# Optimization experiments

Hardware: AMD Instinct MI355X
Metric: run time of the kernel (lower is better)

## Reference

```python
import jax, jax.numpy as jnp
import numpy as np

N_NODES = 32
GAT_OUT = 64
LSTM_H = 128
N_CLS = 4
NEG_SLOPE = 0.2


def setup_inputs() -> dict:
    key = jax.random.key(0)
    ks = jax.random.split(key, 12)
    B, T, E = 32, 512, 96
    F, H = GAT_OUT, LSTM_H
    s = 0.05
    return {
        "x_seq": jax.random.normal(ks[0], (B, T, N_NODES), jnp.float32),
        "edge_index": jax.random.randint(ks[1], (2, E), 0, N_NODES, jnp.int32),
        # GATConv params (heads=1): lin weight [in=1, F], attention vectors [F], bias [F]
        "w_gat": jax.random.normal(ks[2], (1, F), jnp.float32) * s,
        "att_src": jax.random.normal(ks[3], (F,), jnp.float32) * s,
        "att_dst": jax.random.normal(ks[4], (F,), jnp.float32) * s,
        "b_gat": jnp.zeros((F,), jnp.float32),
        # LSTM params, torch gate order (i, f, g, o)
        "W_ih": jax.random.normal(ks[5], (N_NODES * F, 4 * H), jnp.float32) * s,
        "W_hh": jax.random.normal(ks[6], (H, 4 * H), jnp.float32) * s,
        "b_ih": jnp.zeros((4 * H,), jnp.float32),
        "b_hh": jnp.zeros((4 * H,), jnp.float32),
        # classifier
        "W_fc": jax.random.normal(ks[7], (H, N_CLS), jnp.float32) * s,
        "b_fc": jnp.zeros((N_CLS,), jnp.float32),
    }


def _forward(x_seq, edge_index, w_gat, att_src, att_dst, b_gat,
             W_ih, W_hh, b_ih, b_hh, W_fc, b_fc):
    B, T, N = x_seq.shape
    F = w_gat.shape[1]
    H = W_hh.shape[0]

    # --- GAT over all (B,T) steps at once (PyG GATConv, heads=1, self-loops) ---
    loops = jnp.arange(N, dtype=edge_index.dtype)
    src = jnp.concatenate([edge_index[0], loops])  # [Et]
    dst = jnp.concatenate([edge_index[1], loops])  # [Et]
    Et = src.shape[0]

    h = x_seq[..., None] * w_gat            # [B,T,N,F] (in_channels=1 linear)
    a_s = h @ att_src                        # [B,T,N]
    a_d = h @ att_dst                        # [B,T,N]
    e = a_s[..., src] + a_d[..., dst]        # [B,T,Et]
    e = jnp.where(e > 0, e, NEG_SLOPE * e)   # LeakyReLU(0.2)

    # segment softmax over destination node, batched over B*T
    e2 = jnp.moveaxis(e, -1, 0).reshape(Et, B * T)
    m = jax.ops.segment_max(e2, dst, num_segments=N)        # [N,B*T]
    ex = jnp.exp(e2 - m[dst])
    z = jax.ops.segment_sum(ex, dst, num_segments=N)        # [N,B*T]
    alpha = ex / z[dst]                                      # [Et,B*T]
    alpha = jnp.moveaxis(alpha.reshape(Et, B, T), 0, -1)     # [B,T,Et]

    msg = alpha[..., None] * h[:, :, src, :]                 # [B,T,Et,F]
    onehot = (dst[:, None] == jnp.arange(N)).astype(h.dtype)  # [Et,N]
    out = jnp.einsum('btef,en->btnf', msg, onehot) + b_gat    # [B,T,N,F]

    seq = out.reshape(B, T, N * F)           # [B,T,2048]

    # --- single-layer LSTM (batch_first), torch gate order i,f,g,o ---
    xw = seq @ W_ih + (b_ih + b_hh)          # [B,T,4H]

    def step(carry, xw_t):
        hs, cs = carry
        g = xw_t + hs @ W_hh                 # [B,4H]
        i, f, gg, o = jnp.split(g, 4, axis=-1)
        cs = jax.nn.sigmoid(f) * cs + jax.nn.sigmoid(i) * jnp.tanh(gg)
        hs = jax.nn.sigmoid(o) * jnp.tanh(cs)
        return (hs, cs), None

    h0 = jnp.zeros((B, H), seq.dtype)
    (h_last, _), _ = jax.lax.scan(step, (h0, h0), jnp.moveaxis(xw, 1, 0))

    return h_last @ W_fc + b_fc              # [B,num_classes]


def reference(x_seq, edge_index, w_gat, att_src, att_dst, b_gat,
              W_ih, W_hh, b_ih, b_hh, W_fc, b_fc):
    return _forward(x_seq, edge_index, w_gat, att_src, att_dst, b_gat,
                    W_ih, W_hh, b_ih, b_hh, W_fc, b_fc)
```

## Files before the change

### kernel.cpp

```cpp
#include <hip/hip_runtime.h>

#define NN 32
#define FF 64
#define HH 128
#define G4 512
#define BB 32
#define TT 512
#define ET 128
#define NPOS (BB*TT)

__device__ __forceinline__ float frcp(float x) { return __builtin_amdgcn_rcpf(x); }

__global__ __launch_bounds__(512) void prep_kernel(const float* __restrict__ w_gat,
                                                   const float* __restrict__ b_gat,
                                                   const float* __restrict__ W_ih,
                                                   float* __restrict__ W_eff,
                                                   float* __restrict__ biasp) {
  int j = threadIdx.x;
  int n = blockIdx.x;
  float accw = 0.f, accb = 0.f;
#pragma unroll 8
  for (int f = 0; f < FF; ++f) {
    float wv = W_ih[(n * FF + f) * G4 + j];
    accw = fmaf(w_gat[f], wv, accw);
    accb = fmaf(b_gat[f], wv, accb);
  }
  W_eff[n * G4 + j] = accw;
  biasp[n * G4 + j] = accb;
}

__global__ __launch_bounds__(512) void prep2_kernel(const float* __restrict__ biasp,
                                                    const float* __restrict__ b_ih,
                                                    const float* __restrict__ b_hh,
                                                    const float* __restrict__ w_gat,
                                                    const float* __restrict__ att_src,
                                                    const float* __restrict__ att_dst,
                                                    const int* __restrict__ ei,
                                                    float* __restrict__ bias_eff,
                                                    float* __restrict__ scal,
                                                    int* __restrict__ srt_g,
                                                    int* __restrict__ off_g) {
  __shared__ int cnt[NN];
  __shared__ int off[NN + 1];
  __shared__ int srt[ET];
  int j = threadIdx.x;
  if (j < NN) cnt[j] = 0;
  float acc = b_ih[j] + b_hh[j];
#pragma unroll
  for (int n = 0; n < NN; ++n) acc += biasp[n * G4 + j];
  bias_eff[j] = acc;
  if (j == 0) {
    float cs = 0.f, cd = 0.f;
    for (int f = 0; f < FF; ++f) {
      cs = fmaf(w_gat[f], att_src[f], cs);
      cd = fmaf(w_gat[f], att_dst[f], cd);
    }
    scal[0] = cs;
    scal[1] = cd;
  }
  __syncthreads();
  int s = 0, d = 0, tk = 0;
  if (j < ET) {
    if (j < 96) { s = ei[j]; d = ei[96 + j]; }
    else { s = j - 96; d = j - 96; }
    tk = atomicAdd(&cnt[d], 1);
  }
  __syncthreads();
  if (j == 0) {
    off[0] = 0;
    for (int n = 0; n < NN; ++n) off[n + 1] = off[n] + cnt[n];
  }
  __syncthreads();
  if (j < ET) srt[off[d] + tk] = s;
  __syncthreads();
  if (j < ET) srt_g[j] = srt[j];
  if (j < NN + 1) off_g[j] = off[j];
}

__global__ __launch_bounds__(128) void prep3_kernel(const float* __restrict__ W_hh,
                                                    float* __restrict__ Wt) {
  int tid = blockIdx.x;
  int m = threadIdx.x;
  int r = tid >> 2, kq = tid & 3;
  int g = m >> 5, kk = m & 31;
  Wt[tid * 128 + m] = W_hh[(kq * 32 + kk) * G4 + g * 128 + r];
}

__global__ __launch_bounds__(256) void gatxw_kernel(const float* __restrict__ x_seq,
                                                    const int* __restrict__ srt_g,
                                                    const int* __restrict__ off_g,
                                                    const float* __restrict__ scal,
                                                    const float* __restrict__ W_eff,
                                                    const float* __restrict__ bias_eff,
                                                    float* __restrict__ xw) {
  __shared__ int srt[ET];
  __shared__ int offs[NN + 1];
  __shared__ float xs[8 * 32];
  __shared__ float sl[8 * 32];
  int tid = threadIdx.x;
  int posbase = blockIdx.x * 8;
  float we0[NN], we1[NN];
#pragma unroll
  for (int nn = 0; nn < NN; ++nn) {
    we0[nn] = W_eff[nn * G4 + tid];
    we1[nn] = W_eff[nn * G4 + 256 + tid];
  }
  float b0 = bias_eff[tid], b1 = bias_eff[256 + tid];
  if (tid < ET) srt[tid] = srt_g[tid];
  if (tid < NN + 1) offs[tid] = off_g[tid];
  int p = tid >> 5, n = tid & 31;
  xs[tid] = x_seq[posbase * NN + tid];
  __syncthreads();
  float cs = scal[0], cd = scal[1];
  int base = p * 32;
  int e0 = offs[n], e1 = offs[n + 1];
  float xn = xs[base + n];
  float cdxn = cd * xn;
  float m = -3.0e38f;
  for (int e = e0; e < e1; ++e) {
    float ev = fmaf(cs, xs[base + srt[e]], cdxn);
    ev = ev > 0.f ? ev : 0.2f * ev;
    m = fmaxf(m, ev);
  }
  float z = 0.f, sa = 0.f;
  for (int e = e0; e < e1; ++e) {
    float xsv = xs[base + srt[e]];
    float ev = fmaf(cs, xsv, cdxn);
    ev = ev > 0.f ? ev : 0.2f * ev;
    float ex = __expf(ev - m);
    z += ex;
    sa = fmaf(ex, xsv, sa);
  }
  sl[p * 32 + n] = sa * frcp(z);
  __syncthreads();
  for (int pp = 0; pp < 8; ++pp) {
    const float4* sp = (const float4*)&sl[pp * 32];
    float a0 = b0, a1 = b1;
#pragma unroll
    for (int q = 0; q < 8; ++q) {
      float4 sv = sp[q];
      a0 = fmaf(sv.x, we0[4 * q], a0);
      a0 = fmaf(sv.y, we0[4 * q + 1], a0);
      a0 = fmaf(sv.z, we0[4 * q + 2], a0);
      a0 = fmaf(sv.w, we0[4 * q + 3], a0);
      a1 = fmaf(sv.x, we1[4 * q], a1);
      a1 = fmaf(sv.y, we1[4 * q + 1], a1);
      a1 = fmaf(sv.z, we1[4 * q + 2], a1);
      a1 = fmaf(sv.w, we1[4 * q + 3], a1);
    }
    size_t row = (size_t)(posbase + pp) * G4;
    xw[row + tid] = a0;
    xw[row + 256 + tid] = a1;
  }
}


#define PK16F(HP, W0, W1, W2, W3) \
  "v_pk_fma_f32 v[216:217], v[" HP "], v[" W0 "], 0\n\t" \
  "v_pk_fma_f32 v[218:219], v[" HP "], v[" W1 "], 0\n\t" \
  "v_pk_fma_f32 v[220:221], v[" HP "], v[" W2 "], 0\n\t" \
  "v_pk_fma_f32 v[222:223], v[" HP "], v[" W3 "], 0\n\t"

#define PK16A(HP, W0, W1, W2, W3) \
  "v_pk_fma_f32 v[216:217], v[" HP "], v[" W0 "], v[216:217]\n\t" \
  "v_pk_fma_f32 v[218:219], v[" HP "], v[" W1 "], v[218:219]\n\t" \
  "v_pk_fma_f32 v[220:221], v[" HP "], v[" W2 "], v[220:221]\n\t" \
  "v_pk_fma_f32 v[222:223], v[" HP "], v[" W3 "], v[222:223]\n\t"

#define PHASE(XSLOT, RD, WR) \
  "ds_read_b128 v[32:35], " RD "\n\t" \
  "ds_read_b128 v[36:39], " RD " offset:16\n\t" \
  "ds_read_b128 v[40:43], " RD " offset:32\n\t" \
  "ds_read_b128 v[44:47], " RD " offset:48\n\t" \
  "ds_read_b128 v[48:51], " RD " offset:64\n\t" \
  "ds_read_b128 v[52:55], " RD " offset:80\n\t" \
  "ds_read_b128 v[56:59], " RD " offset:96\n\t" \
  "ds_read_b128 v[60:63], " RD " offset:112\n\t" \
  "s_waitcnt vmcnt(3)\n\t" \
  "v_mov_b32 v215, " XSLOT "\n\t" \
  "global_load_dword " XSLOT ", v194, %[xwb]\n\t" \
  "v_add_u32 v194, 0x800, v194\n\t" \
  "s_waitcnt lgkmcnt(7)\n\t" \
  PK16F("32:33", "64:65",  "96:97",   "128:129", "160:161") \
  PK16A("34:35", "66:67",  "98:99",   "130:131", "162:163") \
  "s_waitcnt lgkmcnt(6)\n\t" \
  PK16A("36:37", "68:69",  "100:101", "132:133", "164:165") \
  PK16A("38:39", "70:71",  "102:103", "134:135", "166:167") \
  "s_waitcnt lgkmcnt(5)\n\t" \
  PK16A("40:41", "72:73",  "104:105", "136:137", "168:169") \
  PK16A("42:43", "74:75",  "106:107", "138:139", "170:171") \
  "s_waitcnt lgkmcnt(4)\n\t" \
  PK16A("44:45", "76:77",  "108:109", "140:141", "172:173") \
  PK16A("46:47", "78:79",  "110:111", "142:143", "174:175") \
  "s_waitcnt lgkmcnt(3)\n\t" \
  PK16A("48:49", "80:81",  "112:113", "144:145", "176:177") \
  PK16A("50:51", "82:83",  "114:115", "146:147", "178:179") \
  "s_waitcnt lgkmcnt(2)\n\t" \
  PK16A("52:53", "84:85",  "116:117", "148:149", "180:181") \
  PK16A("54:55", "86:87",  "118:119", "150:151", "182:183") \
  "s_waitcnt lgkmcnt(1)\n\t" \
  PK16A("56:57", "88:89",  "120:121", "152:153", "184:185") \
  PK16A("58:59", "90:91",  "122:123", "154:155", "186:187") \
  "s_waitcnt lgkmcnt(0)\n\t" \
  PK16A("60:61", "92:93",  "124:125", "156:157", "188:189") \
  PK16A("62:63", "94:95",  "126:127", "158:159", "190:191") \
  "v_add_f32 v204, v216, v217\n\t" \
  "v_add_f32 v205, v218, v219\n\t" \
  "v_add_f32 v206, v220, v221\n\t" \
  "v_add_f32 v207, v222, v223\n\t" \
  "v_fmac_f32 v204, v215, v200\n\t" \
  "v_fmac_f32 v205, v215, v201\n\t" \
  "v_fmac_f32 v206, v215, v202\n\t" \
  "v_fmac_f32 v207, v215, v203\n\t" \
  "v_add_f32_dpp v204, v204, v204 quad_perm:[1,0,3,2] row_mask:0xf bank_mask:0xf\n\t" \
  "v_add_f32_dpp v205, v205, v205 quad_perm:[1,0,3,2] row_mask:0xf bank_mask:0xf\n\t" \
  "v_add_f32_dpp v206, v206, v206 quad_perm:[1,0,3,2] row_mask:0xf bank_mask:0xf\n\t" \
  "v_add_f32_dpp v207, v207, v207 quad_perm:[1,0,3,2] row_mask:0xf bank_mask:0xf\n\t" \
  "v_add_f32_dpp v204, v204, v204 quad_perm:[2,3,0,1] row_mask:0xf bank_mask:0xf\n\t" \
  "v_add_f32_dpp v205, v205, v205 quad_perm:[2,3,0,1] row_mask:0xf bank_mask:0xf\n\t" \
  "v_add_f32_dpp v206, v206, v206 quad_perm:[2,3,0,1] row_mask:0xf bank_mask:0xf\n\t" \
  "v_add_f32_dpp v207, v207, v207 quad_perm:[2,3,0,1] row_mask:0xf bank_mask:0xf\n\t" \
  "v_mul_f32 v208, 0xbfb8aa3b, v204\n\t" \
  "v_mul_f32 v209, 0xbfb8aa3b, v205\n\t" \
  "v_mul_f32 v210, 0x4038aa3b, v206\n\t" \
  "v_mul_f32 v211, 0xbfb8aa3b, v207\n\t" \
  "v_exp_f32 v208, v208\n\t" \
  "v_exp_f32 v209, v209\n\t" \
  "v_exp_f32 v210, v210\n\t" \
  "v_exp_f32 v211, v211\n\t" \
  "v_add_f32 v208, 1.0, v208\n\t" \
  "v_add_f32 v209, 1.0, v209\n\t" \
  "v_add_f32 v210, 1.0, v210\n\t" \
  "v_add_f32 v211, 1.0, v211\n\t" \
  "v_rcp_f32 v208, v208\n\t" \
  "v_rcp_f32 v209, v209\n\t" \
  "v_rcp_f32 v210, v210\n\t" \
  "v_rcp_f32 v211, v211\n\t" \
  "v_fma_f32 v210, -2.0, v210, 1.0\n\t" \
  "v_mul_f32 v212, v208, v210\n\t" \
  "v_fma_f32 v199, v209, v199, v212\n\t" \
  "v_mul_f32 v214, 0x4038aa3b, v199\n\t" \
  "v_exp_f32 v214, v214\n\t" \
  "s_nop 1\n\t" \
  "v_add_f32 v214, 1.0, v214\n\t" \
  "v_rcp_f32 v214, v214\n\t" \
  "s_nop 1\n\t" \
  "v_fma_f32 v214, -2.0, v214, 1.0\n\t" \
  "v_mul_f32 v213, v211, v214\n\t" \
  "ds_write_b32 " WR ", v213\n\t" \
  "s_waitcnt lgkmcnt(0)\n\t" \
  "s_barrier\n\t"

__global__ __launch_bounds__(512, 2) void lstm_kernel(const float* __restrict__ xw,
                                                      const float* __restrict__ Wt,
                                                      const float* __restrict__ W_fc,
                                                      const float* __restrict__ b_fc,
                                                      float* __restrict__ out) {
  __shared__ __align__(16) float lds[320];
  int b = blockIdx.x, tid = threadIdx.x;
  int r = tid >> 2, kq = tid & 3;
  if (tid < 320) lds[tid] = 0.f;
  const float* xwb = xw + (size_t)b * TT * G4;
  unsigned xoff0 = (unsigned)((kq * 128 + r) * 4);
  unsigned wtoff = (unsigned)(tid * 512);
  unsigned lbase = (unsigned)(uintptr_t)&lds[0];
  unsigned rda = lbase + kq * 160;
  unsigned rdb = rda + 640;
  unsigned wra = lbase + (((r >> 5) * 40 + (r & 31)) << 2);
  unsigned wrb = wra + 640;
  float mh0 = (kq == 0) ? 1.f : 0.f;
  float mh1 = (kq == 1) ? 1.f : 0.f;
  float mh2 = (kq == 2) ? 1.f : 0.f;
  float mh3 = (kq == 3) ? 1.f : 0.f;
  __syncthreads();
  asm volatile(
    "v_mov_b32 v194, %[xo]\n\t"
    "v_mov_b32 v195, %[rda]\n\t"
    "v_mov_b32 v196, %[rdb]\n\t"
    "v_mov_b32 v197, %[wra]\n\t"
    "v_mov_b32 v198, %[wrb]\n\t"
    "v_mov_b32 v199, 0\n\t"
    "v_mov_b32 v200, %[m0]\n\t"
    "v_mov_b32 v201, %[m1]\n\t"
    "v_mov_b32 v202, %[m2]\n\t"
    "v_mov_b32 v203, %[m3]\n\t"
    "global_load_dword v224, v194, %[xwb]\n\t"
    "v_add_u32 v194, 0x800, v194\n\t"
    "global_load_dword v225, v194, %[xwb]\n\t"
    "v_add_u32 v194, 0x800, v194\n\t"
    "global_load_dword v226, v194, %[xwb]\n\t"
    "v_add_u32 v194, 0x800, v194\n\t"
    "global_load_dword v227, v194, %[xwb]\n\t"
    "v_add_u32 v194, 0x800, v194\n\t"
    "global_load_dwordx4 v[64:67], %[wto], %[wtb] offset:0\n\t"
    "global_load_dwordx4 v[68:71], %[wto], %[wtb] offset:16\n\t"
    "global_load_dwordx4 v[72:75], %[wto], %[wtb] offset:32\n\t"
    "global_load_dwordx4 v[76:79], %[wto], %[wtb] offset:48\n\t"
    "global_load_dwordx4 v[80:83], %[wto], %[wtb] offset:64\n\t"
    "global_load_dwordx4 v[84:87], %[wto], %[wtb] offset:80\n\t"
    "global_load_dwordx4 v[88:91], %[wto], %[wtb] offset:96\n\t"
    "global_load_dwordx4 v[92:95], %[wto], %[wtb] offset:112\n\t"
    "global_load_dwordx4 v[96:99], %[wto], %[wtb] offset:128\n\t"
    "global_load_dwordx4 v[100:103], %[wto], %[wtb] offset:144\n\t"
    "global_load_dwordx4 v[104:107], %[wto], %[wtb] offset:160\n\t"
    "global_load_dwordx4 v[108:111], %[wto], %[wtb] offset:176\n\t"
    "global_load_dwordx4 v[112:115], %[wto], %[wtb] offset:192\n\t"
    "global_load_dwordx4 v[116:119], %[wto], %[wtb] offset:208\n\t"
    "global_load_dwordx4 v[120:123], %[wto], %[wtb] offset:224\n\t"
    "global_load_dwordx4 v[124:127], %[wto], %[wtb] offset:240\n\t"
    "global_load_dwordx4 v[128:131], %[wto], %[wtb] offset:256\n\t"
    "global_load_dwordx4 v[132:135], %[wto], %[wtb] offset:272\n\t"
    "global_load_dwordx4 v[136:139], %[wto], %[wtb] offset:288\n\t"
    "global_load_dwordx4 v[140:143], %[wto], %[wtb] offset:304\n\t"
    "global_load_dwordx4 v[144:147], %[wto], %[wtb] offset:320\n\t"
    "global_load_dwordx4 v[148:151], %[wto], %[wtb] offset:336\n\t"
    "global_load_dwordx4 v[152:155], %[wto], %[wtb] offset:352\n\t"
    "global_load_dwordx4 v[156:159], %[wto], %[wtb] offset:368\n\t"
    "global_load_dwordx4 v[160:163], %[wto], %[wtb] offset:384\n\t"
    "global_load_dwordx4 v[164:167], %[wto], %[wtb] offset:400\n\t"
    "global_load_dwordx4 v[168:171], %[wto], %[wtb] offset:416\n\t"
    "global_load_dwordx4 v[172:175], %[wto], %[wtb] offset:432\n\t"
    "global_load_dwordx4 v[176:179], %[wto], %[wtb] offset:448\n\t"
    "global_load_dwordx4 v[180:183], %[wto], %[wtb] offset:464\n\t"
    "global_load_dwordx4 v[184:187], %[wto], %[wtb] offset:480\n\t"
    "global_load_dwordx4 v[188:191], %[wto], %[wtb] offset:496\n\t"
    "s_waitcnt vmcnt(4)\n\t"
    "s_movk_i32 s20, 0x80\n\t"
    "L_lstm_%=:\n\t"
    PHASE("v224", "v195", "v198")
    PHASE("v225", "v196", "v197")
    PHASE("v226", "v195", "v198")
    PHASE("v227", "v196", "v197")
    "s_sub_u32 s20, s20, 1\n\t"
    "s_cmp_lg_u32 s20, 0\n\t"
    "s_cbranch_scc1 L_lstm_%=\n\t"
    "s_waitcnt vmcnt(0) lgkmcnt(0)\n\t"
    :
    : [xwb]"s"(xwb), [wtb]"s"(Wt), [wto]"v"(wtoff), [xo]"v"(xoff0),
      [rda]"v"(rda), [rdb]"v"(rdb), [wra]"v"(wra), [wrb]"v"(wrb),
      [m0]"v"(mh0), [m1]"v"(mh1), [m2]"v"(mh2), [m3]"v"(mh3)
    : "memory", "scc", "s20",
      "v32","v33","v34","v35","v36","v37","v38","v39",
      "v40","v41","v42","v43","v44","v45","v46","v47",
      "v48","v49","v50","v51","v52","v53","v54","v55",
      "v56","v57","v58","v59","v60","v61","v62","v63",
      "v64","v65","v66","v67","v68","v69","v70","v71",
      "v72","v73","v74","v75","v76","v77","v78","v79",
      "v80","v81","v82","v83","v84","v85","v86","v87",
      "v88","v89","v90","v91","v92","v93","v94","v95",
      "v96","v97","v98","v99","v100","v101","v102","v103",
      "v104","v105","v106","v107","v108","v109","v110","v111",
      "v112","v113","v114","v115","v116","v117","v118","v119",
      "v120","v121","v122","v123","v124","v125","v126","v127",
      "v128","v129","v130","v131","v132","v133","v134","v135",
      "v136","v137","v138","v139","v140","v141","v142","v143",
      "v144","v145","v146","v147","v148","v149","v150","v151",
      "v152","v153","v154","v155","v156","v157","v158","v159",
      "v160","v161","v162","v163","v164","v165","v166","v167",
      "v168","v169","v170","v171","v172","v173","v174","v175",
      "v176","v177","v178","v179","v180","v181","v182","v183",
      "v184","v185","v186","v187","v188","v189","v190","v191",
      "v192","v193","v194","v195","v196","v197","v198","v199",
      "v200","v201","v202","v203","v204","v205","v206","v207",
      "v208","v209","v210","v211","v212","v213","v214","v215",
      "v216","v217","v218","v219","v220","v221","v222","v223",
      "v224","v225","v226","v227");
  __syncthreads();
  if (tid < 4) {
    float acc = b_fc[tid];
#pragma unroll 8
    for (int k = 0; k < HH; ++k)
      acc = fmaf(lds[(k >> 5) * 40 + (k & 31)], W_fc[k * 4 + tid], acc);
    out[b * 4 + tid] = acc;
  }
}

extern "C" void kernel_launch(void* const* d_in, const int* in_sizes, int n_in,
                              void* d_out, int out_size, void* d_ws, size_t ws_size,
                              hipStream_t stream) {
  const float* x_seq   = (const float*)d_in[0];
  const int*   ei      = (const int*)d_in[1];
  const float* w_gat   = (const float*)d_in[2];
  const float* att_src = (const float*)d_in[3];
  const float* att_dst = (const float*)d_in[4];
  const float* b_gat   = (const float*)d_in[5];
  const float* W_ih    = (const float*)d_in[6];
  const float* W_hh    = (const float*)d_in[7];
  const float* b_ih    = (const float*)d_in[8];
  const float* b_hh    = (const float*)d_in[9];
  const float* W_fc    = (const float*)d_in[10];
  const float* b_fc    = (const float*)d_in[11];

  float* ws = (float*)d_ws;
  float* Wt       = ws;
  float* xw       = Wt + 65536;
  float* W_eff    = xw + (size_t)(NPOS + 8) * G4;
  float* bias_eff = W_eff + NN * G4;
  float* scal     = bias_eff + G4;
  float* biasp    = scal + 2;
  int*   srt_g    = (int*)(biasp + NN * G4);
  int*   off_g    = srt_g + ET;

  prep_kernel<<<NN, G4, 0, stream>>>(w_gat, b_gat, W_ih, W_eff, biasp);
  prep2_kernel<<<1, G4, 0, stream>>>(biasp, b_ih, b_hh, w_gat, att_src, att_dst, ei,
                                     bias_eff, scal, srt_g, off_g);
  prep3_kernel<<<G4, 128, 0, stream>>>(W_hh, Wt);
  gatxw_kernel<<<NPOS / 8, 256, 0, stream>>>(x_seq, srt_g, off_g, scal, W_eff, bias_eff, xw);
  lstm_kernel<<<BB, G4, 0, stream>>>(xw, Wt, W_fc, b_fc, (float*)d_out);
}
```

Baseline: 396.1 us.

## Split LSTM K-reduction eight ways per hidden-unit pair and merge prep kernels

The LSTM recurrence now gives each thread two hidden units and an eighth of the K dimension, reduced with three DPP steps, instead of one unit and a quarter of K. This halves the per-thread shared-memory reads of h per step and shortens the serial FMA chain in the latency-bound recurrent loop, at the cost of an extra DPP stage and a reordered W_hh layout. The separate prep2/prep3 kernels are folded into prep_kernel and gatxw_kernel, which removes two launches but makes every gatxw block redo the edge sort, bias sum and attention scalars.

```diff
diff --git a/kernel.cpp b/kernel.cpp
--- a/kernel.cpp
+++ b/kernel.cpp
@@ -14,8 +14,10 @@
 __global__ __launch_bounds__(512) void prep_kernel(const float* __restrict__ w_gat,
                                                    const float* __restrict__ b_gat,
                                                    const float* __restrict__ W_ih,
+                                                   const float* __restrict__ W_hh,
                                                    float* __restrict__ W_eff,
-                                                   float* __restrict__ biasp) {
+                                                   float* __restrict__ biasp,
+                                                   float* __restrict__ Wt) {
   int j = threadIdx.x;
   int n = blockIdx.x;
   float accw = 0.f, accb = 0.f;
@@ -27,76 +29,34 @@
   }
   W_eff[n * G4 + j] = accw;
   biasp[n * G4 + j] = accb;
+  int g0 = (n * G4 + j) * 4;
+#pragma unroll
+  for (int q = 0; q < 4; ++q) {
+    int e = g0 + q;
+    int t = e >> 7, idx = e & 127;
+    int ko = t & 7, r2 = t >> 3;
+    int m = idx >> 4, kk = idx & 15;
+    int col = (m >> 1) * 128 + 2 * r2 + (m & 1);
+    Wt[e] = W_hh[(ko * 16 + kk) * G4 + col];
+  }
 }
 
-__global__ __launch_bounds__(512) void prep2_kernel(const float* __restrict__ biasp,
-                                                    const float* __restrict__ b_ih,
-                                                    const float* __restrict__ b_hh,
+__global__ __launch_bounds__(256) void gatxw_kernel(const float* __restrict__ x_seq,
+                                                    const int* __restrict__ ei,
                                                     const float* __restrict__ w_gat,
                                                     const float* __restrict__ att_src,
                                                     const float* __restrict__ att_dst,
-                                                    const int* __restrict__ ei,
-                                                    float* __restrict__ bias_eff,
-                                                    float* __restrict__ scal,
-                                                    int* __restrict__ srt_g,
-                                                    int* __restrict__ off_g) {
-  __shared__ int cnt[NN];
-  __shared__ int off[NN + 1];
-  __shared__ int srt[ET];
-  int j = threadIdx.x;
-  if (j < NN) cnt[j] = 0;
-  float acc = b_ih[j] + b_hh[j];
-#pragma unroll
-  for (int n = 0; n < NN; ++n) acc += biasp[n * G4 + j];
-  bias_eff[j] = acc;
-  if (j == 0) {
-    float cs = 0.f, cd = 0.f;
-    for (int f = 0; f < FF; ++f) {
-      cs = fmaf(w_gat[f], att_src[f], cs);
-      cd = fmaf(w_gat[f], att_dst[f], cd);
-    }
-    scal[0] = cs;
-    scal[1] = cd;
-  }
-  __syncthreads();
-  int s = 0, d = 0, tk = 0;
-  if (j < ET) {
-    if (j < 96) { s = ei[j]; d = ei[96 + j]; }
-    else { s = j - 96; d = j - 96; }
-    tk = atomicAdd(&cnt[d], 1);
-  }
-  __syncthreads();
-  if (j == 0) {
-    off[0] = 0;
-    for (int n = 0; n < NN; ++n) off[n + 1] = off[n] + cnt[n];
-  }
-  __syncthreads();
-  if (j < ET) srt[off[d] + tk] = s;
-  __syncthreads();
-  if (j < ET) srt_g[j] = srt[j];
-  if (j < NN + 1) off_g[j] = off[j];
-}
-
-__global__ __launch_bounds__(128) void prep3_kernel(const float* __restrict__ W_hh,
-                                                    float* __restrict__ Wt) {
-  int tid = blockIdx.x;
-  int m = threadIdx.x;
-  int r = tid >> 2, kq = tid & 3;
-  int g = m >> 5, kk = m & 31;
-  Wt[tid * 128 + m] = W_hh[(kq * 32 + kk) * G4 + g * 128 + r];
-}
-
-__global__ __launch_bounds__(256) void gatxw_kernel(const float* __restrict__ x_seq,
-                                                    const int* __restrict__ srt_g,
-                                                    const int* __restrict__ off_g,
-                                                    const float* __restrict__ scal,
+                                                    const float* __restrict__ b_ih,
+                                                    const float* __restrict__ b_hh,
                                                     const float* __restrict__ W_eff,
-                                                    const float* __restrict__ bias_eff,
+                                                    const float* __restrict__ biasp,
                                                     float* __restrict__ xw) {
   __shared__ int srt[ET];
   __shared__ int offs[NN + 1];
-  __shared__ float xs[8 * 32];
-  __shared__ float sl[8 * 32];
+  __shared__ int cnt[NN];
+  __shared__ float xs[256];
+  __shared__ float sl[256];
+  __shared__ float scal_sh[2];
   int tid = threadIdx.x;
   int posbase = blockIdx.x * 8;
   float we0[NN], we1[NN];
@@ -105,13 +65,41 @@
     we0[nn] = W_eff[nn * G4 + tid];
     we1[nn] = W_eff[nn * G4 + 256 + tid];
   }
-  float b0 = bias_eff[tid], b1 = bias_eff[256 + tid];
-  if (tid < ET) srt[tid] = srt_g[tid];
-  if (tid < NN + 1) offs[tid] = off_g[tid];
+  float b0 = b_ih[tid] + b_hh[tid];
+  float b1 = b_ih[256 + tid] + b_hh[256 + tid];
+#pragma unroll 8
+  for (int n = 0; n < NN; ++n) {
+    b0 += biasp[n * G4 + tid];
+    b1 += biasp[n * G4 + 256 + tid];
+  }
+  if (tid < NN) cnt[tid] = 0;
+  __syncthreads();
+  int es = 0, ed = 0, tk = 0;
+  if (tid < ET) {
+    if (tid < 96) { es = ei[tid]; ed = ei[96 + tid]; }
+    else { es = tid - 96; ed = tid - 96; }
+    tk = atomicAdd(&cnt[ed], 1);
+  }
+  __syncthreads();
+  if (tid == 0) {
+    offs[0] = 0;
+    for (int n = 0; n < NN; ++n) offs[n + 1] = offs[n] + cnt[n];
+  }
+  if (tid == 1) {
+    float cs = 0.f, cd = 0.f;
+    for (int f = 0; f < FF; ++f) {
+      cs = fmaf(w_gat[f], att_src[f], cs);
+      cd = fmaf(w_gat[f], att_dst[f], cd);
+    }
+    scal_sh[0] = cs;
+    scal_sh[1] = cd;
+  }
+  __syncthreads();
+  if (tid < ET) srt[offs[ed] + tk] = es;
+  xs[tid] = x_seq[posbase * NN + tid];
+  __syncthreads();
+  float cs = scal_sh[0], cd = scal_sh[1];
   int p = tid >> 5, n = tid & 31;
-  xs[tid] = x_seq[posbase * NN + tid];
-  __syncthreads();
-  float cs = scal[0], cd = scal[1];
   int base = p * 32;
   int e0 = offs[n], e1 = offs[n + 1];
   float xn = xs[base + n];
@@ -155,99 +143,129 @@
 }
 
 
-#define PK16F(HP, W0, W1, W2, W3) \
-  "v_pk_fma_f32 v[216:217], v[" HP "], v[" W0 "], 0\n\t" \
-  "v_pk_fma_f32 v[218:219], v[" HP "], v[" W1 "], 0\n\t" \
-  "v_pk_fma_f32 v[220:221], v[" HP "], v[" W2 "], 0\n\t" \
-  "v_pk_fma_f32 v[222:223], v[" HP "], v[" W3 "], 0\n\t"
-
-#define PK16A(HP, W0, W1, W2, W3) \
-  "v_pk_fma_f32 v[216:217], v[" HP "], v[" W0 "], v[216:217]\n\t" \
-  "v_pk_fma_f32 v[218:219], v[" HP "], v[" W1 "], v[218:219]\n\t" \
-  "v_pk_fma_f32 v[220:221], v[" HP "], v[" W2 "], v[220:221]\n\t" \
-  "v_pk_fma_f32 v[222:223], v[" HP "], v[" W3 "], v[222:223]\n\t"
+#define PK8F(HP, W0, W1, W2, W3, W4, W5, W6, W7) \
+  "v_pk_fma_f32 v[48:49], v[" HP "], v[" W0 "], 0\n\t" \
+  "v_pk_fma_f32 v[50:51], v[" HP "], v[" W1 "], 0\n\t" \
+  "v_pk_fma_f32 v[52:53], v[" HP "], v[" W2 "], 0\n\t" \
+  "v_pk_fma_f32 v[54:55], v[" HP "], v[" W3 "], 0\n\t" \
+  "v_pk_fma_f32 v[56:57], v[" HP "], v[" W4 "], 0\n\t" \
+  "v_pk_fma_f32 v[58:59], v[" HP "], v[" W5 "], 0\n\t" \
+  "v_pk_fma_f32 v[60:61], v[" HP "], v[" W6 "], 0\n\t" \
+  "v_pk_fma_f32 v[62:63], v[" HP "], v[" W7 "], 0\n\t"
+
+#define PK8A(HP, W0, W1, W2, W3, W4, W5, W6, W7) \
+  "v_pk_fma_f32 v[48:49], v[" HP "], v[" W0 "], v[48:49]\n\t" \
+  "v_pk_fma_f32 v[50:51], v[" HP "], v[" W1 "], v[50:51]\n\t" \
+  "v_pk_fma_f32 v[52:53], v[" HP "], v[" W2 "], v[52:53]\n\t" \
+  "v_pk_fma_f32 v[54:55], v[" HP "], v[" W3 "], v[54:55]\n\t" \
+  "v_pk_fma_f32 v[56:57], v[" HP "], v[" W4 "], v[56:57]\n\t" \
+  "v_pk_fma_f32 v[58:59], v[" HP "], v[" W5 "], v[58:59]\n\t" \
+  "v_pk_fma_f32 v[60:61], v[" HP "], v[" W6 "], v[60:61]\n\t" \
+  "v_pk_fma_f32 v[62:63], v[" HP "], v[" W7 "], v[62:63]\n\t"
+
+#define DPP8(CTRL) \
+  "v_add_f32_dpp v208, v208, v208 " CTRL " row_mask:0xf bank_mask:0xf\n\t" \
+  "v_add_f32_dpp v209, v209, v209 " CTRL " row_mask:0xf bank_mask:0xf\n\t" \
+  "v_add_f32_dpp v210, v210, v210 " CTRL " row_mask:0xf bank_mask:0xf\n\t" \
+  "v_add_f32_dpp v211, v211, v211 " CTRL " row_mask:0xf bank_mask:0xf\n\t" \
+  "v_add_f32_dpp v212, v212, v212 " CTRL " row_mask:0xf bank_mask:0xf\n\t" \
+  "v_add_f32_dpp v213, v213, v213 " CTRL " row_mask:0xf bank_mask:0xf\n\t" \
+  "v_add_f32_dpp v214, v214, v214 " CTRL " row_mask:0xf bank_mask:0xf\n\t" \
+  "v_add_f32_dpp v215, v215, v215 " CTRL " row_mask:0xf bank_mask:0xf\n\t"
 
 #define PHASE(XSLOT, RD, WR) \
   "ds_read_b128 v[32:35], " RD "\n\t" \
   "ds_read_b128 v[36:39], " RD " offset:16\n\t" \
   "ds_read_b128 v[40:43], " RD " offset:32\n\t" \
   "ds_read_b128 v[44:47], " RD " offset:48\n\t" \
-  "ds_read_b128 v[48:51], " RD " offset:64\n\t" \
-  "ds_read_b128 v[52:55], " RD " offset:80\n\t" \
-  "ds_read_b128 v[56:59], " RD " offset:96\n\t" \
-  "ds_read_b128 v[60:63], " RD " offset:112\n\t" \
   "s_waitcnt vmcnt(3)\n\t" \
-  "v_mov_b32 v215, " XSLOT "\n\t" \
+  "v_mov_b32 v192, " XSLOT "\n\t" \
   "global_load_dword " XSLOT ", v194, %[xwb]\n\t" \
   "v_add_u32 v194, 0x800, v194\n\t" \
-  "s_waitcnt lgkmcnt(7)\n\t" \
-  PK16F("32:33", "64:65",  "96:97",   "128:129", "160:161") \
-  PK16A("34:35", "66:67",  "98:99",   "130:131", "162:163") \
-  "s_waitcnt lgkmcnt(6)\n\t" \
-  PK16A("36:37", "68:69",  "100:101", "132:133", "164:165") \
-  PK16A("38:39", "70:71",  "102:103", "134:135", "166:167") \
-  "s_waitcnt lgkmcnt(5)\n\t" \
-  PK16A("40:41", "72:73",  "104:105", "136:137", "168:169") \
-  PK16A("42:43", "74:75",  "106:107", "138:139", "170:171") \
-  "s_waitcnt lgkmcnt(4)\n\t" \
-  PK16A("44:45", "76:77",  "108:109", "140:141", "172:173") \
-  PK16A("46:47", "78:79",  "110:111", "142:143", "174:175") \
   "s_waitcnt lgkmcnt(3)\n\t" \
-  PK16A("48:49", "80:81",  "112:113", "144:145", "176:177") \
-  PK16A("50:51", "82:83",  "114:115", "146:147", "178:179") \
+  PK8F("32:33", "64:65", "80:81", "96:97", "112:113", "128:129", "144:145", "160:161", "176:177") \
+  PK8A("34:35", "66:67", "82:83", "98:99", "114:115", "130:131", "146:147", "162:163", "178:179") \
   "s_waitcnt lgkmcnt(2)\n\t" \
-  PK16A("52:53", "84:85",  "116:117", "148:149", "180:181") \
-  PK16A("54:55", "86:87",  "118:119", "150:151", "182:183") \
+  PK8A("36:37", "68:69", "84:85", "100:101", "116:117", "132:133", "148:149", "164:165", "180:181") \
+  PK8A("38:39", "70:71", "86:87", "102:103", "118:119", "134:135", "150:151", "166:167", "182:183") \
   "s_waitcnt lgkmcnt(1)\n\t" \
-  PK16A("56:57", "88:89",  "120:121", "152:153", "184:185") \
-  PK16A("58:59", "90:91",  "122:123", "154:155", "186:187") \
+  PK8A("40:41", "72:73", "88:89", "104:105", "120:121", "136:137", "152:153", "168:169", "184:185") \
+  PK8A("42:43", "74:75", "90:91", "106:107", "122:123", "138:139", "154:155", "170:171", "186:187") \
   "s_waitcnt lgkmcnt(0)\n\t" \
-  PK16A("60:61", "92:93",  "124:125", "156:157", "188:189") \
-  PK16A("62:63", "94:95",  "126:127", "158:159", "190:191") \
-  "v_add_f32 v204, v216, v217\n\t" \
-  "v_add_f32 v205, v218, v219\n\t" \
-  "v_add_f32 v206, v220, v221\n\t" \
-  "v_add_f32 v207, v222, v223\n\t" \
-  "v_fmac_f32 v204, v215, v200\n\t" \
-  "v_fmac_f32 v205, v215, v201\n\t" \
-  "v_fmac_f32 v206, v215, v202\n\t" \
-  "v_fmac_f32 v207, v215, v203\n\t" \
-  "v_add_f32_dpp v204, v204, v204 quad_perm:[1,0,3,2] row_mask:0xf bank_mask:0xf\n\t" \
-  "v_add_f32_dpp v205, v205, v205 quad_perm:[1,0,3,2] row_mask:0xf bank_mask:0xf\n\t" \
-  "v_add_f32_dpp v206, v206, v206 quad_perm:[1,0,3,2] row_mask:0xf bank_mask:0xf\n\t" \
-  "v_add_f32_dpp v207, v207, v207 quad_perm:[1,0,3,2] row_mask:0xf bank_mask:0xf\n\t" \
-  "v_add_f32_dpp v204, v204, v204 quad_perm:[2,3,0,1] row_mask:0xf bank_mask:0xf\n\t" \
-  "v_add_f32_dpp v205, v205, v205 quad_perm:[2,3,0,1] row_mask:0xf bank_mask:0xf\n\t" \
-  "v_add_f32_dpp v206, v206, v206 quad_perm:[2,3,0,1] row_mask:0xf bank_mask:0xf\n\t" \
-  "v_add_f32_dpp v207, v207, v207 quad_perm:[2,3,0,1] row_mask:0xf bank_mask:0xf\n\t" \
-  "v_mul_f32 v208, 0xbfb8aa3b, v204\n\t" \
-  "v_mul_f32 v209, 0xbfb8aa3b, v205\n\t" \
-  "v_mul_f32 v210, 0x4038aa3b, v206\n\t" \
-  "v_mul_f32 v211, 0xbfb8aa3b, v207\n\t" \
-  "v_exp_f32 v208, v208\n\t" \
-  "v_exp_f32 v209, v209\n\t" \
-  "v_exp_f32 v210, v210\n\t" \
-  "v_exp_f32 v211, v211\n\t" \
-  "v_add_f32 v208, 1.0, v208\n\t" \
-  "v_add_f32 v209, 1.0, v209\n\t" \
-  "v_add_f32 v210, 1.0, v210\n\t" \
-  "v_add_f32 v211, 1.0, v211\n\t" \
-  "v_rcp_f32 v208, v208\n\t" \
-  "v_rcp_f32 v209, v209\n\t" \
-  "v_rcp_f32 v210, v210\n\t" \
-  "v_rcp_f32 v211, v211\n\t" \
-  "v_fma_f32 v210, -2.0, v210, 1.0\n\t" \
-  "v_mul_f32 v212, v208, v210\n\t" \
-  "v_fma_f32 v199, v209, v199, v212\n\t" \
-  "v_mul_f32 v214, 0x4038aa3b, v199\n\t" \
-  "v_exp_f32 v214, v214\n\t" \
+  PK8A("44:45", "76:77", "92:93", "108:109", "124:125", "140:141", "156:157", "172:173", "188:189") \
+  PK8A("46:47", "78:79", "94:95", "110:111", "126:127", "142:143", "158:159", "174:175", "190:191") \
+  "v_add_f32 v208, v48, v49\n\t" \
+  "v_add_f32 v209, v50, v51\n\t" \
+  "v_add_f32 v210, v52, v53\n\t" \
+  "v_add_f32 v211, v54, v55\n\t" \
+  "v_add_f32 v212, v56, v57\n\t" \
+  "v_add_f32 v213, v58, v59\n\t" \
+  "v_add_f32 v214, v60, v61\n\t" \
+  "v_add_f32 v215, v62, v63\n\t" \
+  "v_fmac_f32 v208, v192, v200\n\t" \
+  "v_fmac_f32 v209, v192, v201\n\t" \
+  "v_fmac_f32 v210, v192, v202\n\t" \
+  "v_fmac_f32 v211, v192, v203\n\t" \
+  "v_fmac_f32 v212, v192, v204\n\t" \
+  "v_fmac_f32 v213, v192, v205\n\t" \
+  "v_fmac_f32 v214, v192, v206\n\t" \
+  "v_fmac_f32 v215, v192, v207\n\t" \
+  DPP8("quad_perm:[1,0,3,2]") \
+  DPP8("quad_perm:[2,3,0,1]") \
+  DPP8("row_half_mirror") \
+  "v_mul_f32 v48, 0xbfb8aa3b, v208\n\t" \
+  "v_mul_f32 v49, 0xbfb8aa3b, v209\n\t" \
+  "v_mul_f32 v50, 0xbfb8aa3b, v210\n\t" \
+  "v_mul_f32 v51, 0xbfb8aa3b, v211\n\t" \
+  "v_mul_f32 v52, 0x4038aa3b, v212\n\t" \
+  "v_mul_f32 v53, 0x4038aa3b, v213\n\t" \
+  "v_mul_f32 v54, 0xbfb8aa3b, v214\n\t" \
+  "v_mul_f32 v55, 0xbfb8aa3b, v215\n\t" \
+  "v_exp_f32 v48, v48\n\t" \
+  "v_exp_f32 v49, v49\n\t" \
+  "v_exp_f32 v50, v50\n\t" \
+  "v_exp_f32 v51, v51\n\t" \
+  "v_exp_f32 v52, v52\n\t" \
+  "v_exp_f32 v53, v53\n\t" \
+  "v_exp_f32 v54, v54\n\t" \
+  "v_exp_f32 v55, v55\n\t" \
+  "v_add_f32 v48, 1.0, v48\n\t" \
+  "v_add_f32 v49, 1.0, v49\n\t" \
+  "v_add_f32 v50, 1.0, v50\n\t" \
+  "v_add_f32 v51, 1.0, v51\n\t" \
+  "v_add_f32 v52, 1.0, v52\n\t" \
+  "v_add_f32 v53, 1.0, v53\n\t" \
+  "v_add_f32 v54, 1.0, v54\n\t" \
+  "v_add_f32 v55, 1.0, v55\n\t" \
+  "v_rcp_f32 v48, v48\n\t" \
+  "v_rcp_f32 v49, v49\n\t" \
+  "v_rcp_f32 v50, v50\n\t" \
+  "v_rcp_f32 v51, v51\n\t" \
+  "v_rcp_f32 v52, v52\n\t" \
+  "v_rcp_f32 v53, v53\n\t" \
+  "v_rcp_f32 v54, v54\n\t" \
+  "v_rcp_f32 v55, v55\n\t" \
+  "v_fma_f32 v52, -2.0, v52, 1.0\n\t" \
+  "v_fma_f32 v53, -2.0, v53, 1.0\n\t" \
+  "v_mul_f32 v56, v48, v52\n\t" \
+  "v_mul_f32 v57, v49, v53\n\t" \
+  "v_fma_f32 v199, v50, v199, v56\n\t" \
+  "v_fma_f32 v193, v51, v193, v57\n\t" \
+  "v_mul_f32 v58, 0x4038aa3b, v199\n\t" \
+  "v_mul_f32 v59, 0x4038aa3b, v193\n\t" \
+  "v_exp_f32 v58, v58\n\t" \
+  "v_exp_f32 v59, v59\n\t" \
   "s_nop 1\n\t" \
-  "v_add_f32 v214, 1.0, v214\n\t" \
-  "v_rcp_f32 v214, v214\n\t" \
+  "v_add_f32 v58, 1.0, v58\n\t" \
+  "v_add_f32 v59, 1.0, v59\n\t" \
+  "v_rcp_f32 v58, v58\n\t" \
+  "v_rcp_f32 v59, v59\n\t" \
   "s_nop 1\n\t" \
-  "v_fma_f32 v214, -2.0, v214, 1.0\n\t" \
-  "v_mul_f32 v213, v211, v214\n\t" \
-  "ds_write_b32 " WR ", v213\n\t" \
+  "v_fma_f32 v58, -2.0, v58, 1.0\n\t" \
+  "v_fma_f32 v59, -2.0, v59, 1.0\n\t" \
+  "v_mul_f32 v60, v54, v58\n\t" \
+  "v_mul_f32 v61, v55, v59\n\t" \
+  "ds_write_b64 " WR ", v[60:61]\n\t" \
   "s_waitcnt lgkmcnt(0)\n\t" \
   "s_barrier\n\t"
 
@@ -258,20 +276,24 @@
                                                       float* __restrict__ out) {
   __shared__ __align__(16) float lds[320];
   int b = blockIdx.x, tid = threadIdx.x;
-  int r = tid >> 2, kq = tid & 3;
+  int r2 = tid >> 3, ko = tid & 7;
   if (tid < 320) lds[tid] = 0.f;
   const float* xwb = xw + (size_t)b * TT * G4;
-  unsigned xoff0 = (unsigned)((kq * 128 + r) * 4);
+  unsigned xoff0 = (unsigned)((((ko >> 1) * 128) + 2 * r2 + (ko & 1)) * 4);
   unsigned wtoff = (unsigned)(tid * 512);
   unsigned lbase = (unsigned)(uintptr_t)&lds[0];
-  unsigned rda = lbase + kq * 160;
+  unsigned rda = lbase + (unsigned)(ko * 80);
   unsigned rdb = rda + 640;
-  unsigned wra = lbase + (((r >> 5) * 40 + (r & 31)) << 2);
+  unsigned wra = lbase + (unsigned)((((2 * r2) >> 4) * 20 + ((2 * r2) & 15)) * 4);
   unsigned wrb = wra + 640;
-  float mh0 = (kq == 0) ? 1.f : 0.f;
-  float mh1 = (kq == 1) ? 1.f : 0.f;
-  float mh2 = (kq == 2) ? 1.f : 0.f;
-  float mh3 = (kq == 3) ? 1.f : 0.f;
+  float mh0 = (ko == 0) ? 1.f : 0.f;
+  float mh1 = (ko == 1) ? 1.f : 0.f;
+  float mh2 = (ko == 2) ? 1.f : 0.f;
+  float mh3 = (ko == 3) ? 1.f : 0.f;
+  float mh4 = (ko == 4) ? 1.f : 0.f;
+  float mh5 = (ko == 5) ? 1.f : 0.f;
+  float mh6 = (ko == 6) ? 1.f : 0.f;
+  float mh7 = (ko == 7) ? 1.f : 0.f;
   __syncthreads();
   asm volatile(
     "v_mov_b32 v194, %[xo]\n\t"
@@ -280,10 +302,15 @@
     "v_mov_b32 v197, %[wra]\n\t"
     "v_mov_b32 v198, %[wrb]\n\t"
     "v_mov_b32 v199, 0\n\t"
+    "v_mov_b32 v193, 0\n\t"
     "v_mov_b32 v200, %[m0]\n\t"
     "v_mov_b32 v201, %[m1]\n\t"
     "v_mov_b32 v202, %[m2]\n\t"
     "v_mov_b32 v203, %[m3]\n\t"
+    "v_mov_b32 v204, %[m4]\n\t"
+    "v_mov_b32 v205, %[m5]\n\t"
+    "v_mov_b32 v206, %[m6]\n\t"
+    "v_mov_b32 v207, %[m7]\n\t"
     "global_load_dword v224, v194, %[xwb]\n\t"
     "v_add_u32 v194, 0x800, v194\n\t"
     "global_load_dword v225, v194, %[xwb]\n\t"
@@ -324,7 +351,7 @@
     "global_load_dwordx4 v[180:183], %[wto], %[wtb] offset:464\n\t"
     "global_load_dwordx4 v[184:187], %[wto], %[wtb] offset:480\n\t"
     "global_load_dwordx4 v[188:191], %[wto], %[wtb] offset:496\n\t"
-    "s_waitcnt vmcnt(4)\n\t"
+    "s_waitcnt vmcnt(0)\n\t"
     "s_movk_i32 s20, 0x80\n\t"
     "L_lstm_%=:\n\t"
     PHASE("v224", "v195", "v198")
@@ -338,7 +365,8 @@
     :
     : [xwb]"s"(xwb), [wtb]"s"(Wt), [wto]"v"(wtoff), [xo]"v"(xoff0),
       [rda]"v"(rda), [rdb]"v"(rdb), [wra]"v"(wra), [wrb]"v"(wrb),
-      [m0]"v"(mh0), [m1]"v"(mh1), [m2]"v"(mh2), [m3]"v"(mh3)
+      [m0]"v"(mh0), [m1]"v"(mh1), [m2]"v"(mh2), [m3]"v"(mh3),
+      [m4]"v"(mh4), [m5]"v"(mh5), [m6]"v"(mh6), [m7]"v"(mh7)
     : "memory", "scc", "s20",
       "v32","v33","v34","v35","v36","v37","v38","v39",
       "v40","v41","v42","v43","v44","v45","v46","v47",
@@ -370,7 +398,7 @@
     float acc = b_fc[tid];
 #pragma unroll 8
     for (int k = 0; k < HH; ++k)
-      acc = fmaf(lds[(k >> 5) * 40 + (k & 31)], W_fc[k * 4 + tid], acc);
+      acc = fmaf(lds[(k >> 4) * 20 + (k & 15)], W_fc[k * 4 + tid], acc);
     out[b * 4 + tid] = acc;
   }
 }
@@ -392,19 +420,13 @@
   const float* b_fc    = (const float*)d_in[11];
 
   float* ws = (float*)d_ws;
-  float* Wt       = ws;
-  float* xw       = Wt + 65536;
-  float* W_eff    = xw + (size_t)(NPOS + 8) * G4;
-  float* bias_eff = W_eff + NN * G4;
-  float* scal     = bias_eff + G4;
-  float* biasp    = scal + 2;
-  int*   srt_g    = (int*)(biasp + NN * G4);
-  int*   off_g    = srt_g + ET;
-
-  prep_kernel<<<NN, G4, 0, stream>>>(w_gat, b_gat, W_ih, W_eff, biasp);
-  prep2_kernel<<<1, G4, 0, stream>>>(biasp, b_ih, b_hh, w_gat, att_src, att_dst, ei,
-                                     bias_eff, scal, srt_g, off_g);
-  prep3_kernel<<<G4, 128, 0, stream>>>(W_hh, Wt);
-  gatxw_kernel<<<NPOS / 8, 256, 0, stream>>>(x_seq, srt_g, off_g, scal, W_eff, bias_eff, xw);
+  float* Wt    = ws;
+  float* xw    = Wt + 65536;
+  float* W_eff = xw + (size_t)(NPOS + 8) * G4;
+  float* biasp = W_eff + NN * G4;
+
+  prep_kernel<<<NN, G4, 0, stream>>>(w_gat, b_gat, W_ih, W_hh, W_eff, biasp, Wt);
+  gatxw_kernel<<<NPOS / 8, 256, 0, stream>>>(x_seq, ei, w_gat, att_src, att_dst,
+                                             b_ih, b_hh, W_eff, biasp, xw);
   lstm_kernel<<<BB, G4, 0, stream>>>(xw, Wt, W_fc, b_fc, (float*)d_out);
 }
```

Result: slower. 495.9 us (+25.2%).
